# Kernel optimization log

Hardware: AMD Instinct MI355X
Metric: run time of the kernel (lower is better)

Reference implementation:

```python
import jax, jax.numpy as jnp
import numpy as np

B, T, N, D, K = 8, 64, 512, 64, 8
d = D // K  # per-head dim
NEG = -(2.0 ** 15) + 1.0  # -32767, as in source


def setup_inputs() -> dict:
    key = jax.random.key(0)
    ks = jax.random.split(key, 12)
    s = 0.05
    inp = {
        "x": jax.random.normal(ks[0], (B, T, N, D), dtype=jnp.float32),
        "ste": jax.random.normal(ks[1], (B, T, N, D), dtype=jnp.float32),
        "Wq": jax.random.normal(ks[2], (2 * D, D), dtype=jnp.float32) * s,
        "bq": jnp.zeros((D,), dtype=jnp.float32),
        "Wk": jax.random.normal(ks[3], (2 * D, D), dtype=jnp.float32) * s,
        "bk": jnp.zeros((D,), dtype=jnp.float32),
        "Wv": jax.random.normal(ks[4], (2 * D, D), dtype=jnp.float32) * s,
        "bv": jnp.zeros((D,), dtype=jnp.float32),
        "W1": jax.random.normal(ks[5], (D, D), dtype=jnp.float32) * s,
        "b1": jnp.zeros((D,), dtype=jnp.float32),
        "W2": jax.random.normal(ks[6], (D, D), dtype=jnp.float32) * s,
        "b2": jnp.zeros((D,), dtype=jnp.float32),
    }
    return inp


def reference(x, ste, Wq, bq, Wk, bk, Wv, bv, W1, b1, W2, b2):
    h = jnp.concatenate([x, ste], axis=-1)  # (B,T,N,2D)
    q = jax.nn.relu(jnp.einsum("btnf,fd->btnd", h, Wq) + bq)
    k = jax.nn.relu(jnp.einsum("btnf,fd->btnd", h, Wk) + bk)
    v = jax.nn.relu(jnp.einsum("btnf,fd->btnd", h, Wv) + bv)
    # split D into K heads of size d (torch split/cat over batch == head axis)
    q = q.reshape(B, T, N, K, d)
    k = k.reshape(B, T, N, K, d)
    v = v.reshape(B, T, N, K, d)
    scores = jnp.einsum("btnkd,bsnkd->bnkts", q, k) / jnp.sqrt(jnp.float32(d))
    causal = jnp.tril(jnp.ones((T, T), dtype=bool))  # (T,T)
    scores = jnp.where(causal, scores, jnp.float32(NEG))
    attn = jax.nn.softmax(scores, axis=-1)  # (B,N,K,T,T)
    out = jnp.einsum("bnkts,bsnkd->btnkd", attn, v).reshape(B, T, N, D)
    out = jax.nn.relu(jnp.einsum("btnd,de->btne", out, W1) + b1)
    out = jnp.einsum("btnd,de->btne", out, W2) + b2
    return out
```

## Files before the change

### kernel.cpp

```cpp
#include <hip/hip_runtime.h>


#define Bb 8
#define Tt 64
#define Nn 512
#define Dd 64

typedef unsigned short u16;
typedef unsigned int u32;
typedef __bf16 bf16x8 __attribute__((ext_vector_type(8)));
typedef float f32x4 __attribute__((ext_vector_type(4)));
typedef short s16x8 __attribute__((ext_vector_type(8)));
typedef u32 u32x4 __attribute__((ext_vector_type(4)));

#define QS 72

#define WSQ 0
#define WSK 8192
#define WSV 16384
#define WS1 24576
#define WS2 28672

__device__ inline u16 f2bf(float f) {
    u32 x = __float_as_uint(f);
    x += 0x7fffu + ((x >> 16) & 1u);
    return (u16)(x >> 16);
}
__device__ inline bf16x8 ldf(const u16* p) { return *(const bf16x8*)p; }
__device__ inline bf16x8 zf8() {
    s16x8 z = {0, 0, 0, 0, 0, 0, 0, 0};
    return __builtin_bit_cast(bf16x8, z);
}
__device__ inline bf16x8 pack8(float4 a, float4 b) {
    s16x8 r;
    r[0] = (short)f2bf(a.x); r[1] = (short)f2bf(a.y);
    r[2] = (short)f2bf(a.z); r[3] = (short)f2bf(a.w);
    r[4] = (short)f2bf(b.x); r[5] = (short)f2bf(b.y);
    r[6] = (short)f2bf(b.z); r[7] = (short)f2bf(b.w);
    return __builtin_bit_cast(bf16x8, r);
}
__device__ inline int kperm(int row) {
    return (row & 0x23) | ((row & 4) << 2) | ((row & 0x18) >> 1);
}

template<int KD, int MODE, bool AREG>
__device__ inline void gemm(const bf16x8* afr,
                            const u16* aLds, int As,
                            const u16* __restrict__ WtG,
                            const float* __restrict__ bias,
                            u16* O, int Os, float* G,
                            int w, int lane, float scale) {
    const int l15 = lane & 15, qd = lane >> 4;
    f32x4 acc[4] = {{0,0,0,0},{0,0,0,0},{0,0,0,0},{0,0,0,0}};
#pragma unroll
    for (int c = 0; c < KD / 32; ++c) {
        bf16x8 af = AREG ? afr[c]
                         : ldf(&aLds[(16 * w + l15) * As + c * 32 + qd * 8]);
#pragma unroll
        for (int ct = 0; ct < 4; ++ct) {
            bf16x8 bfr = *(const bf16x8*)&WtG[(16 * ct + l15) * KD + c * 32 + qd * 8];
            acc[ct] = __builtin_amdgcn_mfma_f32_16x16x32_bf16(af, bfr, acc[ct], 0, 0, 0);
        }
    }
#pragma unroll
    for (int ct = 0; ct < 4; ++ct) {
        const int col = 16 * ct + l15;
        const float bv = bias[col];
        if (MODE == 1) {
            ushort4 st;
            st.x = f2bf(fmaxf(acc[ct][0] + bv, 0.f) * scale);
            st.y = f2bf(fmaxf(acc[ct][1] + bv, 0.f) * scale);
            st.z = f2bf(fmaxf(acc[ct][2] + bv, 0.f) * scale);
            st.w = f2bf(fmaxf(acc[ct][3] + bv, 0.f) * scale);
            *(ushort4*)&O[col * Os + 16 * w + 4 * qd] = st;
        } else {
#pragma unroll
            for (int r = 0; r < 4; ++r) {
                const int row = 16 * w + 4 * qd + r;
                float v = acc[ct][r] + bv;
                if (MODE != 2) v = fmaxf(v, 0.f);
                v *= scale;
                if (MODE == 0)      O[row * Os + col] = f2bf(v);
                else if (MODE == 3) O[kperm(row) * Os + col] = f2bf(v);
                else                G[(size_t)row * (Nn * Dd) + col] = v;
            }
        }
    }
}

__global__ __launch_bounds__(256)
void prep_w(const float* __restrict__ Wq, const float* __restrict__ Wk,
            const float* __restrict__ Wv, const float* __restrict__ W1,
            const float* __restrict__ W2, u16* __restrict__ ws) {
    int i = blockIdx.x * 256 + threadIdx.x;
    if (i < 24576) {
        int m = i >> 13;
        int r = i & 8191;
        int k = r >> 6, c = r & 63;
        const float* W = (m == 0) ? Wq : (m == 1) ? Wk : Wv;
        ws[m * 8192 + c * 128 + k] = f2bf(W[r]);
    } else if (i < 32768) {
        int j = i - 24576;
        int m = j >> 12;
        int r = j & 4095;
        int k = r >> 6, c = r & 63;
        const float* W = (m == 0) ? W1 : W2;
        ws[24576 + m * 4096 + c * 64 + k] = f2bf(W[r]);
    }
}

__global__ __launch_bounds__(256, 4)
void ta_fused_kernel(const float* __restrict__ x,  const float* __restrict__ ste,
                     const float* __restrict__ bq, const float* __restrict__ bk,
                     const float* __restrict__ bv, const float* __restrict__ b1,
                     const float* __restrict__ b2, const u16* __restrict__ ws,
                     float* __restrict__ out) {
    __shared__ __align__(16) u16 sm[18432];
    u16* qb = sm;
    u16* kb = sm + 4608;
    u16* vT = sm + 9216;
    u16* ao = sm + 13824;

    const int tid  = threadIdx.x;
    const int w    = tid >> 6;
    const int lane = tid & 63;
    const int l15  = lane & 15, qd = lane >> 4;
    const int bid  = blockIdx.x;
    const int b = bid >> 9, n = bid & 511;

    const int trow = 16 * w + l15;
    const float* xr = x   + (((size_t)b * Tt + trow) * Nn + n) * Dd;
    const float* sr = ste + (((size_t)b * Tt + trow) * Nn + n) * Dd;
    bf16x8 af[4];
#pragma unroll
    for (int c = 0; c < 2; ++c) {
        float4 p0 = *(const float4*)(xr + c * 32 + qd * 8);
        float4 p1 = *(const float4*)(xr + c * 32 + qd * 8 + 4);
        af[c] = pack8(p0, p1);
    }
#pragma unroll
    for (int c = 0; c < 2; ++c) {
        float4 p0 = *(const float4*)(sr + c * 32 + qd * 8);
        float4 p1 = *(const float4*)(sr + c * 32 + qd * 8 + 4);
        af[c + 2] = pack8(p0, p1);
    }

    gemm<128, 0, true>(af, nullptr, 0, ws + WSQ, bq, qb, QS, nullptr, w, lane,
                       0.35355339059327373f);
    gemm<128, 3, true>(af, nullptr, 0, ws + WSK, bk, kb, QS, nullptr, w, lane, 1.f);
    gemm<128, 1, true>(af, nullptr, 0, ws + WSV, bv, vT, QS, nullptr, w, lane, 1.f);
    __syncthreads();

    const bf16x8 z8 = zf8();
    const int ctmax = (w >= 2) ? 3 : 1;
#pragma unroll 1
    for (int h8 = 0; h8 < 64; h8 += 8) {
        bf16x8 qfr = (qd == 0) ? ldf(&qb[(16 * w + l15) * QS + h8]) : z8;
        f32x4 sv[4] = {{0,0,0,0},{0,0,0,0},{0,0,0,0},{0,0,0,0}};
#pragma unroll
        for (int ct = 0; ct < 4; ++ct) {
            if (ct <= ctmax) {
                bf16x8 kfr = (qd == 0) ? ldf(&kb[(16 * ct + l15) * QS + h8]) : z8;
                sv[ct] = __builtin_amdgcn_mfma_f32_16x16x32_bf16(kfr, qfr, sv[ct], 0, 0, 0);
            }
        }
        const int t = 16 * w + l15;
        float dsum = 0.f;
        u32 pk[8];
#pragma unroll
        for (int ct = 0; ct < 4; ++ct) {
            if (ct <= ctmax) {
                const int sbase = 8 * qd + 4 * (ct & 1) + 32 * (ct >> 1);
#pragma unroll
                for (int r = 0; r < 4; ++r) {
                    float e = (sbase + r <= t) ? __expf(sv[ct][r]) : 0.f;
                    sv[ct][r] = e;
                    dsum += e;
                }
                pk[2 * ct]     = (u32)f2bf(sv[ct][0]) | ((u32)f2bf(sv[ct][1]) << 16);
                pk[2 * ct + 1] = (u32)f2bf(sv[ct][2]) | ((u32)f2bf(sv[ct][3]) << 16);
            } else {
                pk[2 * ct] = 0; pk[2 * ct + 1] = 0;
            }
        }
        dsum += __shfl_xor(dsum, 16, 64);
        dsum += __shfl_xor(dsum, 32, 64);

        const int vrow = h8 + (l15 & 7);
        f32x4 o = {0, 0, 0, 0};
        {
            bf16x8 va0 = ldf(&vT[vrow * QS + 0 + qd * 8]);
            u32x4 pb0 = {pk[0], pk[1], pk[2], pk[3]};
            o = __builtin_amdgcn_mfma_f32_16x16x32_bf16(
                    va0, __builtin_bit_cast(bf16x8, pb0), o, 0, 0, 0);
        }
        if (w >= 2) {
            bf16x8 va1 = ldf(&vT[vrow * QS + 32 + qd * 8]);
            u32x4 pb1 = {pk[4], pk[5], pk[6], pk[7]};
            o = __builtin_amdgcn_mfma_f32_16x16x32_bf16(
                    va1, __builtin_bit_cast(bf16x8, pb1), o, 0, 0, 0);
        }
        float invd = __builtin_amdgcn_rcpf(dsum);
        if (qd < 2) {
            ushort4 st;
            st.x = f2bf(o[0] * invd);
            st.y = f2bf(o[1] * invd);
            st.z = f2bf(o[2] * invd);
            st.w = f2bf(o[3] * invd);
            *(ushort4*)&ao[(16 * w + l15) * QS + h8 + 4 * qd] = st;
        }
    }

    u16* abuf = qb;
    gemm<64, 0, false>(nullptr, ao, QS, ws + WS1, b1, abuf, QS, nullptr,
                       w, lane, 1.f);
    float* ob = out + (((size_t)b * Tt) * Nn + n) * Dd;
    gemm<64, 2, false>(nullptr, abuf, QS, ws + WS2, b2, nullptr, 0, ob,
                       w, lane, 1.f);
}

extern "C" void kernel_launch(void* const* d_in, const int* in_sizes, int n_in,
                              void* d_out, int out_size, void* d_ws, size_t ws_size,
                              hipStream_t stream) {
    const float* x   = (const float*)d_in[0];
    const float* ste = (const float*)d_in[1];
    const float* Wq  = (const float*)d_in[2];
    const float* bq  = (const float*)d_in[3];
    const float* Wk  = (const float*)d_in[4];
    const float* bk  = (const float*)d_in[5];
    const float* Wv  = (const float*)d_in[6];
    const float* bv  = (const float*)d_in[7];
    const float* W1  = (const float*)d_in[8];
    const float* b1  = (const float*)d_in[9];
    const float* W2  = (const float*)d_in[10];
    const float* b2  = (const float*)d_in[11];
    float* out = (float*)d_out;
    u16* ws = (u16*)d_ws;

    hipLaunchKernelGGL(prep_w, dim3(128), dim3(256), 0, stream,
                       Wq, Wk, Wv, W1, W2, ws);
    hipLaunchKernelGGL(ta_fused_kernel, dim3(Bb * Nn), dim3(256), 0, stream,
                       x, ste, bq, bk, bv, b1, b2, ws, out);
}
```

Before: 288.6 us.

## Split each block's work across eight waves instead of four

Doubles the block size to 512 threads. Each pair of waves now shares a 16-row tile, and each wave computes half the output columns in the GEMMs and half the heads in the attention loop. The aim is more waves per block to hide memory and MFMA latency, and a lower per-wave register footprint. In exchange, both waves of a pair redundantly load and convert the same x/ste rows, and extra __syncthreads barriers are added between the attention and MLP stages.

```diff
diff --git a/kernel.cpp b/kernel.cpp
--- a/kernel.cpp
+++ b/kernel.cpp
@@ -49,35 +49,37 @@
                             const u16* __restrict__ WtG,
                             const float* __restrict__ bias,
                             u16* O, int Os, float* G,
-                            int w, int lane, float scale) {
+                            int m, int u, int lane, float scale) {
     const int l15 = lane & 15, qd = lane >> 4;
-    f32x4 acc[4] = {{0,0,0,0},{0,0,0,0},{0,0,0,0},{0,0,0,0}};
+    f32x4 acc[2] = {{0,0,0,0},{0,0,0,0}};
 #pragma unroll
     for (int c = 0; c < KD / 32; ++c) {
         bf16x8 af = AREG ? afr[c]
-                         : ldf(&aLds[(16 * w + l15) * As + c * 32 + qd * 8]);
-#pragma unroll
-        for (int ct = 0; ct < 4; ++ct) {
+                         : ldf(&aLds[(16 * m + l15) * As + c * 32 + qd * 8]);
+#pragma unroll
+        for (int j = 0; j < 2; ++j) {
+            const int ct = 2 * u + j;
             bf16x8 bfr = *(const bf16x8*)&WtG[(16 * ct + l15) * KD + c * 32 + qd * 8];
-            acc[ct] = __builtin_amdgcn_mfma_f32_16x16x32_bf16(af, bfr, acc[ct], 0, 0, 0);
-        }
-    }
-#pragma unroll
-    for (int ct = 0; ct < 4; ++ct) {
+            acc[j] = __builtin_amdgcn_mfma_f32_16x16x32_bf16(af, bfr, acc[j], 0, 0, 0);
+        }
+    }
+#pragma unroll
+    for (int j = 0; j < 2; ++j) {
+        const int ct = 2 * u + j;
         const int col = 16 * ct + l15;
         const float bv = bias[col];
         if (MODE == 1) {
             ushort4 st;
-            st.x = f2bf(fmaxf(acc[ct][0] + bv, 0.f) * scale);
-            st.y = f2bf(fmaxf(acc[ct][1] + bv, 0.f) * scale);
-            st.z = f2bf(fmaxf(acc[ct][2] + bv, 0.f) * scale);
-            st.w = f2bf(fmaxf(acc[ct][3] + bv, 0.f) * scale);
-            *(ushort4*)&O[col * Os + 16 * w + 4 * qd] = st;
+            st.x = f2bf(fmaxf(acc[j][0] + bv, 0.f) * scale);
+            st.y = f2bf(fmaxf(acc[j][1] + bv, 0.f) * scale);
+            st.z = f2bf(fmaxf(acc[j][2] + bv, 0.f) * scale);
+            st.w = f2bf(fmaxf(acc[j][3] + bv, 0.f) * scale);
+            *(ushort4*)&O[col * Os + 16 * m + 4 * qd] = st;
         } else {
 #pragma unroll
             for (int r = 0; r < 4; ++r) {
-                const int row = 16 * w + 4 * qd + r;
-                float v = acc[ct][r] + bv;
+                const int row = 16 * m + 4 * qd + r;
+                float v = acc[j][r] + bv;
                 if (MODE != 2) v = fmaxf(v, 0.f);
                 v *= scale;
                 if (MODE == 0)      O[row * Os + col] = f2bf(v);
@@ -109,7 +111,7 @@
     }
 }
 
-__global__ __launch_bounds__(256, 4)
+__global__ __launch_bounds__(512, 8)
 void ta_fused_kernel(const float* __restrict__ x,  const float* __restrict__ ste,
                      const float* __restrict__ bq, const float* __restrict__ bk,
                      const float* __restrict__ bv, const float* __restrict__ b1,
@@ -123,12 +125,14 @@
 
     const int tid  = threadIdx.x;
     const int w    = tid >> 6;
+    const int m    = w >> 1;
+    const int u    = w & 1;
     const int lane = tid & 63;
     const int l15  = lane & 15, qd = lane >> 4;
     const int bid  = blockIdx.x;
     const int b = bid >> 9, n = bid & 511;
 
-    const int trow = 16 * w + l15;
+    const int trow = 16 * m + l15;
     const float* xr = x   + (((size_t)b * Tt + trow) * Nn + n) * Dd;
     const float* sr = ste + (((size_t)b * Tt + trow) * Nn + n) * Dd;
     bf16x8 af[4];
@@ -145,17 +149,18 @@
         af[c + 2] = pack8(p0, p1);
     }
 
-    gemm<128, 0, true>(af, nullptr, 0, ws + WSQ, bq, qb, QS, nullptr, w, lane,
+    gemm<128, 0, true>(af, nullptr, 0, ws + WSQ, bq, qb, QS, nullptr, m, u, lane,
                        0.35355339059327373f);
-    gemm<128, 3, true>(af, nullptr, 0, ws + WSK, bk, kb, QS, nullptr, w, lane, 1.f);
-    gemm<128, 1, true>(af, nullptr, 0, ws + WSV, bv, vT, QS, nullptr, w, lane, 1.f);
+    gemm<128, 3, true>(af, nullptr, 0, ws + WSK, bk, kb, QS, nullptr, m, u, lane, 1.f);
+    gemm<128, 1, true>(af, nullptr, 0, ws + WSV, bv, vT, QS, nullptr, m, u, lane, 1.f);
     __syncthreads();
 
     const bf16x8 z8 = zf8();
-    const int ctmax = (w >= 2) ? 3 : 1;
+    const int ctmax = (m >= 2) ? 3 : 1;
 #pragma unroll 1
-    for (int h8 = 0; h8 < 64; h8 += 8) {
-        bf16x8 qfr = (qd == 0) ? ldf(&qb[(16 * w + l15) * QS + h8]) : z8;
+    for (int i = 0; i < 4; ++i) {
+        const int h8 = 32 * u + 8 * i;
+        bf16x8 qfr = (qd == 0) ? ldf(&qb[(16 * m + l15) * QS + h8]) : z8;
         f32x4 sv[4] = {{0,0,0,0},{0,0,0,0},{0,0,0,0},{0,0,0,0}};
 #pragma unroll
         for (int ct = 0; ct < 4; ++ct) {
@@ -164,7 +169,7 @@
                 sv[ct] = __builtin_amdgcn_mfma_f32_16x16x32_bf16(kfr, qfr, sv[ct], 0, 0, 0);
             }
         }
-        const int t = 16 * w + l15;
+        const int t = 16 * m + l15;
         float dsum = 0.f;
         u32 pk[8];
 #pragma unroll
@@ -194,7 +199,7 @@
             o = __builtin_amdgcn_mfma_f32_16x16x32_bf16(
                     va0, __builtin_bit_cast(bf16x8, pb0), o, 0, 0, 0);
         }
-        if (w >= 2) {
+        if (m >= 2) {
             bf16x8 va1 = ldf(&vT[vrow * QS + 32 + qd * 8]);
             u32x4 pb1 = {pk[4], pk[5], pk[6], pk[7]};
             o = __builtin_amdgcn_mfma_f32_16x16x32_bf16(
@@ -207,16 +212,18 @@
             st.y = f2bf(o[1] * invd);
             st.z = f2bf(o[2] * invd);
             st.w = f2bf(o[3] * invd);
-            *(ushort4*)&ao[(16 * w + l15) * QS + h8 + 4 * qd] = st;
-        }
-    }
+            *(ushort4*)&ao[(16 * m + l15) * QS + h8 + 4 * qd] = st;
+        }
+    }
+    __syncthreads();
 
     u16* abuf = qb;
     gemm<64, 0, false>(nullptr, ao, QS, ws + WS1, b1, abuf, QS, nullptr,
-                       w, lane, 1.f);
+                       m, u, lane, 1.f);
+    __syncthreads();
     float* ob = out + (((size_t)b * Tt) * Nn + n) * Dd;
     gemm<64, 2, false>(nullptr, abuf, QS, ws + WS2, b2, nullptr, 0, ob,
-                       w, lane, 1.f);
+                       m, u, lane, 1.f);
 }
 
 extern "C" void kernel_launch(void* const* d_in, const int* in_sizes, int n_in,
@@ -239,6 +246,6 @@
 
     hipLaunchKernelGGL(prep_w, dim3(128), dim3(256), 0, stream,
                        Wq, Wk, Wv, W1, W2, ws);
-    hipLaunchKernelGGL(ta_fused_kernel, dim3(Bb * Nn), dim3(256), 0, stream,
+    hipLaunchKernelGGL(ta_fused_kernel, dim3(Bb * Nn), dim3(512), 0, stream,
                        x, ste, bq, bk, bv, b1, b2, ws, out);
 }
```

After: 299.5 us. 1.04x slower.

## Process four nodes per block and prefetch next node inputs during compute

Applied to the files above, without the earlier changes.

Each block now loops over four consecutive n positions instead of one, with a quarter as many blocks launched. While the QKV projections for the current node run, the x/ste rows for the next node are loaded into registers, so global load latency overlaps compute. This also spreads launch overhead and weight fetches across more work per block. In exchange each block runs longer, fewer blocks are available to hide latency (1024 blocks), and the prefetch registers add pressure under the 4-blocks-per-CU launch bound. An added barrier before the output GEMMs guards the reuse of shared memory between iterations.

```diff
diff --git a/kernel.cpp b/kernel.cpp
--- a/kernel.cpp
+++ b/kernel.cpp
@@ -5,6 +5,7 @@
 #define Tt 64
 #define Nn 512
 #define Dd 64
+#define NT 4
 
 typedef unsigned short u16;
 typedef unsigned int u32;
@@ -126,97 +127,122 @@
     const int lane = tid & 63;
     const int l15  = lane & 15, qd = lane >> 4;
     const int bid  = blockIdx.x;
-    const int b = bid >> 9, n = bid & 511;
+    const int b  = bid >> 7;
+    const int n0 = (bid & 127) << 2;
 
     const int trow = 16 * w + l15;
-    const float* xr = x   + (((size_t)b * Tt + trow) * Nn + n) * Dd;
-    const float* sr = ste + (((size_t)b * Tt + trow) * Nn + n) * Dd;
+    const float* xr0 = x   + (((size_t)b * Tt + trow) * Nn + n0) * Dd;
+    const float* sr0 = ste + (((size_t)b * Tt + trow) * Nn + n0) * Dd;
+
     bf16x8 af[4];
-#pragma unroll
-    for (int c = 0; c < 2; ++c) {
-        float4 p0 = *(const float4*)(xr + c * 32 + qd * 8);
-        float4 p1 = *(const float4*)(xr + c * 32 + qd * 8 + 4);
-        af[c] = pack8(p0, p1);
-    }
-#pragma unroll
-    for (int c = 0; c < 2; ++c) {
-        float4 p0 = *(const float4*)(sr + c * 32 + qd * 8);
-        float4 p1 = *(const float4*)(sr + c * 32 + qd * 8 + 4);
-        af[c + 2] = pack8(p0, p1);
-    }
-
-    gemm<128, 0, true>(af, nullptr, 0, ws + WSQ, bq, qb, QS, nullptr, w, lane,
-                       0.35355339059327373f);
-    gemm<128, 3, true>(af, nullptr, 0, ws + WSK, bk, kb, QS, nullptr, w, lane, 1.f);
-    gemm<128, 1, true>(af, nullptr, 0, ws + WSV, bv, vT, QS, nullptr, w, lane, 1.f);
-    __syncthreads();
-
-    const bf16x8 z8 = zf8();
-    const int ctmax = (w >= 2) ? 3 : 1;
+    {
+        float4 a0 = *(const float4*)(xr0 + qd * 8);
+        float4 a1 = *(const float4*)(xr0 + qd * 8 + 4);
+        float4 a2 = *(const float4*)(xr0 + 32 + qd * 8);
+        float4 a3 = *(const float4*)(xr0 + 32 + qd * 8 + 4);
+        float4 s0 = *(const float4*)(sr0 + qd * 8);
+        float4 s1 = *(const float4*)(sr0 + qd * 8 + 4);
+        float4 s2 = *(const float4*)(sr0 + 32 + qd * 8);
+        float4 s3 = *(const float4*)(sr0 + 32 + qd * 8 + 4);
+        af[0] = pack8(a0, a1); af[1] = pack8(a2, a3);
+        af[2] = pack8(s0, s1); af[3] = pack8(s2, s3);
+    }
+
+    float4 rx0, rx1, rx2, rx3, rs0, rs1, rs2, rs3;
+
 #pragma unroll 1
-    for (int h8 = 0; h8 < 64; h8 += 8) {
-        bf16x8 qfr = (qd == 0) ? ldf(&qb[(16 * w + l15) * QS + h8]) : z8;
-        f32x4 sv[4] = {{0,0,0,0},{0,0,0,0},{0,0,0,0},{0,0,0,0}};
-#pragma unroll
-        for (int ct = 0; ct < 4; ++ct) {
-            if (ct <= ctmax) {
-                bf16x8 kfr = (qd == 0) ? ldf(&kb[(16 * ct + l15) * QS + h8]) : z8;
-                sv[ct] = __builtin_amdgcn_mfma_f32_16x16x32_bf16(kfr, qfr, sv[ct], 0, 0, 0);
-            }
-        }
-        const int t = 16 * w + l15;
-        float dsum = 0.f;
-        u32 pk[8];
-#pragma unroll
-        for (int ct = 0; ct < 4; ++ct) {
-            if (ct <= ctmax) {
-                const int sbase = 8 * qd + 4 * (ct & 1) + 32 * (ct >> 1);
-#pragma unroll
-                for (int r = 0; r < 4; ++r) {
-                    float e = (sbase + r <= t) ? __expf(sv[ct][r]) : 0.f;
-                    sv[ct][r] = e;
-                    dsum += e;
+    for (int it = 0; it < NT; ++it) {
+        gemm<128, 0, true>(af, nullptr, 0, ws + WSQ, bq, qb, QS, nullptr, w, lane,
+                           0.35355339059327373f);
+        gemm<128, 3, true>(af, nullptr, 0, ws + WSK, bk, kb, QS, nullptr, w, lane, 1.f);
+        gemm<128, 1, true>(af, nullptr, 0, ws + WSV, bv, vT, QS, nullptr, w, lane, 1.f);
+        if (it < NT - 1) {
+            const float* xr = xr0 + (it + 1) * Dd;
+            const float* sr = sr0 + (it + 1) * Dd;
+            rx0 = *(const float4*)(xr + qd * 8);
+            rx1 = *(const float4*)(xr + qd * 8 + 4);
+            rx2 = *(const float4*)(xr + 32 + qd * 8);
+            rx3 = *(const float4*)(xr + 32 + qd * 8 + 4);
+            rs0 = *(const float4*)(sr + qd * 8);
+            rs1 = *(const float4*)(sr + qd * 8 + 4);
+            rs2 = *(const float4*)(sr + 32 + qd * 8);
+            rs3 = *(const float4*)(sr + 32 + qd * 8 + 4);
+        }
+        __syncthreads();
+
+        const bf16x8 z8 = zf8();
+        const int ctmax = (w >= 2) ? 3 : 1;
+#pragma unroll 1
+        for (int h8 = 0; h8 < 64; h8 += 8) {
+            bf16x8 qfr = (qd == 0) ? ldf(&qb[(16 * w + l15) * QS + h8]) : z8;
+            f32x4 sv[4] = {{0,0,0,0},{0,0,0,0},{0,0,0,0},{0,0,0,0}};
+#pragma unroll
+            for (int ct = 0; ct < 4; ++ct) {
+                if (ct <= ctmax) {
+                    bf16x8 kfr = (qd == 0) ? ldf(&kb[(16 * ct + l15) * QS + h8]) : z8;
+                    sv[ct] = __builtin_amdgcn_mfma_f32_16x16x32_bf16(kfr, qfr, sv[ct], 0, 0, 0);
                 }
-                pk[2 * ct]     = (u32)f2bf(sv[ct][0]) | ((u32)f2bf(sv[ct][1]) << 16);
-                pk[2 * ct + 1] = (u32)f2bf(sv[ct][2]) | ((u32)f2bf(sv[ct][3]) << 16);
-            } else {
-                pk[2 * ct] = 0; pk[2 * ct + 1] = 0;
-            }
-        }
-        dsum += __shfl_xor(dsum, 16, 64);
-        dsum += __shfl_xor(dsum, 32, 64);
-
-        const int vrow = h8 + (l15 & 7);
-        f32x4 o = {0, 0, 0, 0};
-        {
-            bf16x8 va0 = ldf(&vT[vrow * QS + 0 + qd * 8]);
-            u32x4 pb0 = {pk[0], pk[1], pk[2], pk[3]};
-            o = __builtin_amdgcn_mfma_f32_16x16x32_bf16(
-                    va0, __builtin_bit_cast(bf16x8, pb0), o, 0, 0, 0);
-        }
-        if (w >= 2) {
-            bf16x8 va1 = ldf(&vT[vrow * QS + 32 + qd * 8]);
-            u32x4 pb1 = {pk[4], pk[5], pk[6], pk[7]};
-            o = __builtin_amdgcn_mfma_f32_16x16x32_bf16(
-                    va1, __builtin_bit_cast(bf16x8, pb1), o, 0, 0, 0);
-        }
-        float invd = __builtin_amdgcn_rcpf(dsum);
-        if (qd < 2) {
-            ushort4 st;
-            st.x = f2bf(o[0] * invd);
-            st.y = f2bf(o[1] * invd);
-            st.z = f2bf(o[2] * invd);
-            st.w = f2bf(o[3] * invd);
-            *(ushort4*)&ao[(16 * w + l15) * QS + h8 + 4 * qd] = st;
-        }
-    }
-
-    u16* abuf = qb;
-    gemm<64, 0, false>(nullptr, ao, QS, ws + WS1, b1, abuf, QS, nullptr,
-                       w, lane, 1.f);
-    float* ob = out + (((size_t)b * Tt) * Nn + n) * Dd;
-    gemm<64, 2, false>(nullptr, abuf, QS, ws + WS2, b2, nullptr, 0, ob,
-                       w, lane, 1.f);
+            }
+            const int t = 16 * w + l15;
+            float dsum = 0.f;
+            u32 pk[8];
+#pragma unroll
+            for (int ct = 0; ct < 4; ++ct) {
+                if (ct <= ctmax) {
+                    const int sbase = 8 * qd + 4 * (ct & 1) + 32 * (ct >> 1);
+#pragma unroll
+                    for (int r = 0; r < 4; ++r) {
+                        float e = (sbase + r <= t) ? __expf(sv[ct][r]) : 0.f;
+                        sv[ct][r] = e;
+                        dsum += e;
+                    }
+                    pk[2 * ct]     = (u32)f2bf(sv[ct][0]) | ((u32)f2bf(sv[ct][1]) << 16);
+                    pk[2 * ct + 1] = (u32)f2bf(sv[ct][2]) | ((u32)f2bf(sv[ct][3]) << 16);
+                } else {
+                    pk[2 * ct] = 0; pk[2 * ct + 1] = 0;
+                }
+            }
+            dsum += __shfl_xor(dsum, 16, 64);
+            dsum += __shfl_xor(dsum, 32, 64);
+
+            const int vrow = h8 + (l15 & 7);
+            f32x4 o = {0, 0, 0, 0};
+            {
+                bf16x8 va0 = ldf(&vT[vrow * QS + 0 + qd * 8]);
+                u32x4 pb0 = {pk[0], pk[1], pk[2], pk[3]};
+                o = __builtin_amdgcn_mfma_f32_16x16x32_bf16(
+                        va0, __builtin_bit_cast(bf16x8, pb0), o, 0, 0, 0);
+            }
+            if (w >= 2) {
+                bf16x8 va1 = ldf(&vT[vrow * QS + 32 + qd * 8]);
+                u32x4 pb1 = {pk[4], pk[5], pk[6], pk[7]};
+                o = __builtin_amdgcn_mfma_f32_16x16x32_bf16(
+                        va1, __builtin_bit_cast(bf16x8, pb1), o, 0, 0, 0);
+            }
+            float invd = __builtin_amdgcn_rcpf(dsum);
+            if (qd < 2) {
+                ushort4 st;
+                st.x = f2bf(o[0] * invd);
+                st.y = f2bf(o[1] * invd);
+                st.z = f2bf(o[2] * invd);
+                st.w = f2bf(o[3] * invd);
+                *(ushort4*)&ao[(16 * w + l15) * QS + h8 + 4 * qd] = st;
+            }
+        }
+        __syncthreads();
+
+        u16* abuf = qb;
+        gemm<64, 0, false>(nullptr, ao, QS, ws + WS1, b1, abuf, QS, nullptr,
+                           w, lane, 1.f);
+        float* ob = out + (((size_t)b * Tt) * Nn + (n0 + it)) * Dd;
+        gemm<64, 2, false>(nullptr, abuf, QS, ws + WS2, b2, nullptr, 0, ob,
+                           w, lane, 1.f);
+
+        if (it < NT - 1) {
+            af[0] = pack8(rx0, rx1); af[1] = pack8(rx2, rx3);
+            af[2] = pack8(rs0, rs1); af[3] = pack8(rs2, rs3);
+        }
+    }
 }
 
 extern "C" void kernel_launch(void* const* d_in, const int* in_sizes, int n_in,
@@ -239,6 +265,6 @@
 
     hipLaunchKernelGGL(prep_w, dim3(128), dim3(256), 0, stream,
                        Wq, Wk, Wv, W1, W2, ws);
-    hipLaunchKernelGGL(ta_fused_kernel, dim3(Bb * Nn), dim3(256), 0, stream,
+    hipLaunchKernelGGL(ta_fused_kernel, dim3(Bb * Nn / NT), dim3(256), 0, stream,
                        x, ste, bq, bk, bv, b1, b2, ws, out);
 }
```

Result: slower. 490.9 us (+70.1%).
